# Kernel optimization log

Measured on AMD Instinct MI355X. Metric: run time of the kernel, lower is better.

## Reference

```python
import jax
jax.config.update("jax_enable_x64", True)
import jax.numpy as jnp
import numpy as np

_N = 100000
_E = 6400000


def _mix(z):
    # splitmix64 finalizer: strong per-element mixing so that summing mixed
    # neighbor colors is a (collision-resistant) commutative multiset hash.
    z = z + jnp.uint64(0x9E3779B97F4A7C15)
    z = (z ^ (z >> jnp.uint64(30))) * jnp.uint64(0xBF58476D1CE4E5B9)
    z = (z ^ (z >> jnp.uint64(27))) * jnp.uint64(0x94D049BB133111EB)
    return z ^ (z >> jnp.uint64(31))


def setup_inputs() -> dict:
    key = jax.random.key(0)
    k1, k2 = jax.random.split(key)
    x = jax.random.randint(k1, (_N,), 0, 50, dtype=jnp.int64)
    edge_index = jax.random.randint(k2, (2, _E), 0, _N, dtype=jnp.int64)
    return {"x": x, "edge_index": edge_index}


def reference(x, edge_index):
    # WL refinement: new_color[i] = ID( (x[i], multiset{x[j] : j in N(i)}) ),
    # IDs assigned in first-seen node order (matches the torch hashmap).
    # The torch code sorts neighbors before hashing, so the result depends
    # only on the neighbor MULTISET; we hash the multiset commutatively via
    # sum of splitmix64-mixed colors (collisions negligible in uint64).
    n = x.shape[0]
    row, col = edge_index[0], edge_index[1]  # neighbors of i: row[e] where col[e]==i
    neigh_hash = jax.ops.segment_sum(_mix(x[row].astype(jnp.uint64)), col,
                                     num_segments=n)  # (n,) uint64
    own = _mix(x.astype(jnp.uint64) ^ jnp.uint64(0xABCD1234DEADBEEF))
    sig = _mix(own + neigh_hash)  # (n,) per-node signature

    # Dedup + relabel in first-occurrence order (deterministic, jit-safe).
    _, inv = jnp.unique(sig, return_inverse=True, size=n, fill_value=jnp.uint64(0))
    inv = inv.reshape(-1)
    first = jax.ops.segment_min(jnp.arange(n, dtype=jnp.int64), inv,
                                num_segments=n)  # first node index per group
    rank = jnp.argsort(jnp.argsort(first))  # group -> first-seen color id
    return rank[inv].astype(jnp.int64)
```

## Files before the change

kernel.cpp:

```cpp
#include <hip/hip_runtime.h>

typedef unsigned long long u64;
typedef unsigned int u32;
typedef unsigned short u16;
typedef unsigned char u8;

#define CAP (1 << 18)
#define CAP_MASK (CAP - 1)
#define EMPTY_KEY 0xFFFFFFFFFFFFFFFFULL

#define TILE 8192
#define NXCD 8
#define NBUCK 196
#define BSHIFT 9
#define BMASK 511
#define CAPB 4608

__device__ __forceinline__ u64 mix64(u64 z) {
    z += 0x9E3779B97F4A7C15ULL;
    z = (z ^ (z >> 30)) * 0xBF58476D1CE4E5B9ULL;
    z = (z ^ (z >> 27)) * 0x94D049BB133111EBULL;
    return z ^ (z >> 31);
}

__global__ void init_ws(u64* __restrict__ neigh, u64* __restrict__ keys,
                        u32* __restrict__ firsts, u32* __restrict__ nodeslot,
                        u32* __restrict__ partials, u32* __restrict__ cursor,
                        u8* __restrict__ xb, const int* __restrict__ x, int n) {
    int i = blockIdx.x * blockDim.x + threadIdx.x;
    keys[i] = EMPTY_KEY;
    firsts[i] = 0xFFFFFFFFu;
    if (i < n) { neigh[i] = 0ULL; nodeslot[i] = 0u; xb[i] = (u8)x[i]; }
    if (i < 512) partials[i] = 0u;
    if (i < NXCD * NBUCK) cursor[i] = 0u;
}

__global__ void scatter_edges(const int* __restrict__ row, const int* __restrict__ col,
                              const u8* __restrict__ xb, u32* __restrict__ cursor,
                              u16* __restrict__ bdata, int E, int n) {
    __shared__ u32 ent[TILE];
    __shared__ u32 lcnt[NBUCK];
    __shared__ u32 lscan[NBUCK];
    __shared__ u32 lbase[NBUCK];
    __shared__ u32 s[512];
    int tid = threadIdx.x;
    int g = blockIdx.x & (NXCD - 1);
    long tile0 = (long)blockIdx.x * TILE;
    if (tid < NBUCK) lcnt[tid] = 0u;
    __syncthreads();

    u32 pk_[16];
    u32 nm = (u32)n - 1u;
    #pragma unroll
    for (int k = 0; k < 4; ++k) {
        long e0 = tile0 + (long)k * 2048 + tid * 4;
        u32 pk0 = 0xFFFFFFFFu, pk1 = 0xFFFFFFFFu, pk2 = 0xFFFFFFFFu, pk3 = 0xFFFFFFFFu;
        if (e0 < (long)E) {
            int4 r4 = *(const int4*)(row + e0);
            int4 c4 = *(const int4*)(col + e0);
            u32 c0 = min((u32)c4.x, nm), c1 = min((u32)c4.y, nm);
            u32 c2 = min((u32)c4.z, nm), c3 = min((u32)c4.w, nm);
            u32 v0 = xb[min((u32)r4.x, nm)] & 63u, v1 = xb[min((u32)r4.y, nm)] & 63u;
            u32 v2 = xb[min((u32)r4.z, nm)] & 63u, v3 = xb[min((u32)r4.w, nm)] & 63u;
            pk0 = ((c0 >> BSHIFT) << 16) | ((c0 & BMASK) << 6) | v0;
            pk1 = ((c1 >> BSHIFT) << 16) | ((c1 & BMASK) << 6) | v1;
            pk2 = ((c2 >> BSHIFT) << 16) | ((c2 & BMASK) << 6) | v2;
            pk3 = ((c3 >> BSHIFT) << 16) | ((c3 & BMASK) << 6) | v3;
            atomicAdd(&lcnt[pk0 >> 16], 1u);
            atomicAdd(&lcnt[pk1 >> 16], 1u);
            atomicAdd(&lcnt[pk2 >> 16], 1u);
            atomicAdd(&lcnt[pk3 >> 16], 1u);
        }
        pk_[k * 4 + 0] = pk0; pk_[k * 4 + 1] = pk1;
        pk_[k * 4 + 2] = pk2; pk_[k * 4 + 3] = pk3;
    }
    __syncthreads();

    u32 v = (tid < NBUCK) ? lcnt[tid] : 0u;
    s[tid] = v;
    __syncthreads();
    for (int d = 1; d < 512; d <<= 1) {
        u32 a = (tid >= d) ? s[tid - d] : 0u;
        __syncthreads();
        s[tid] += a;
        __syncthreads();
    }
    if (tid < NBUCK) {
        lscan[tid] = s[tid] - v;
        if (v) lbase[tid] = atomicAdd(&cursor[g * NBUCK + tid], v);
        lcnt[tid] = 0u;
    }
    __syncthreads();

    #pragma unroll
    for (int k = 0; k < 16; ++k) {
        u32 pk = pk_[k];
        if (pk != 0xFFFFFFFFu) {
            u32 b = pk >> 16;
            u32 pos = lscan[b] + atomicAdd(&lcnt[b], 1u);
            ent[pos] = pk;
        }
    }
    __syncthreads();

    int valid = (int)min((long)TILE, (long)E - tile0);
    for (int j = tid; j < valid; j += 512) {
        u32 pk = ent[j];
        u32 b = pk >> 16;
        u32 dst = lbase[b] + ((u32)j - lscan[b]);
        if (dst < CAPB)
            bdata[((size_t)g * NBUCK + b) * CAPB + dst] = (u16)pk;
    }
}

__global__ void bucket_reduce(const u32* __restrict__ cursor, const u16* __restrict__ bdata,
                              u64* __restrict__ neigh, int n) {
    int b = blockIdx.x;
    __shared__ u64 acc[512];
    __shared__ u64 mtab[64];
    int tid = threadIdx.x;
    if (tid < 64) mtab[tid] = mix64((u64)tid);
    if (tid < 512) acc[tid] = 0ULL;
    __syncthreads();
    for (int g = 0; g < NXCD; ++g) {
        u32 cnt = min(cursor[g * NBUCK + b], (u32)CAPB);
        const u16* seg = bdata + ((size_t)g * NBUCK + b) * CAPB;
        for (u32 i = tid; i < cnt; i += 1024) {
            u32 p = (u32)seg[i];
            atomicAdd(&acc[(p >> 6) & 511u], mtab[p & 63u]);
        }
    }
    __syncthreads();
    if (tid < 512) {
        int node = b * 512 + tid;
        if (node < n) neigh[node] = acc[tid];
    }
}

__global__ void edge_kernel(const int* __restrict__ row, const int* __restrict__ col,
                            const int* __restrict__ x, u64* __restrict__ neigh,
                            int nedges, int n) {
    int t = blockIdx.x * blockDim.x + threadIdx.x;
    int e = t * 4;
    u32 nm = (u32)n - 1u;
    if (e + 3 < nedges) {
        int4 r4 = *(const int4*)(row + e);
        int4 c4 = *(const int4*)(col + e);
        u32 r0 = min((u32)r4.x, nm), c0 = min((u32)c4.x, nm);
        u32 r1 = min((u32)r4.y, nm), c1 = min((u32)c4.y, nm);
        u32 r2 = min((u32)r4.z, nm), c2 = min((u32)c4.z, nm);
        u32 r3 = min((u32)r4.w, nm), c3 = min((u32)c4.w, nm);
        atomicAdd(&neigh[c0], mix64((u64)(u32)x[r0]));
        atomicAdd(&neigh[c1], mix64((u64)(u32)x[r1]));
        atomicAdd(&neigh[c2], mix64((u64)(u32)x[r2]));
        atomicAdd(&neigh[c3], mix64((u64)(u32)x[r3]));
    } else {
        for (int k = e; k < nedges; ++k) {
            u32 r = min((u32)row[k], nm);
            u32 c = min((u32)col[k], nm);
            atomicAdd(&neigh[c], mix64((u64)(u32)x[r]));
        }
    }
}

__global__ void sig_insert(const int* __restrict__ x, const u64* __restrict__ neigh,
                           u64* __restrict__ keys, u32* __restrict__ firsts,
                           u32* __restrict__ nodeslot, int n, int half) {
    int i = blockIdx.x * blockDim.x + threadIdx.x;
    int j = i + half;
    bool va = (i < half);
    bool vb = (j < n);
    u64 sa = 0, sb = 0;
    u32 ha = 0, hb = 0;
    if (va) {
        u64 own = mix64(((u64)(u32)x[i]) ^ 0xABCD1234DEADBEEFULL);
        sa = mix64(own + neigh[i]);
        ha = (u32)(sa ^ (sa >> 32)) & CAP_MASK;
    }
    if (vb) {
        u64 own = mix64(((u64)(u32)x[j]) ^ 0xABCD1234DEADBEEFULL);
        sb = mix64(own + neigh[j]);
        hb = (u32)(sb ^ (sb >> 32)) & CAP_MASK;
    }
    bool da = !va, db = !vb;
    for (int p = 0; p < CAP && !(da && db); ++p) {
        u64 oa, ob;
        if (!da) oa = atomicCAS(&keys[ha], EMPTY_KEY, sa);
        if (!db) ob = atomicCAS(&keys[hb], EMPTY_KEY, sb);
        if (!da) { if (oa == EMPTY_KEY || oa == sa) da = true; else ha = (ha + 1) & CAP_MASK; }
        if (!db) { if (ob == EMPTY_KEY || ob == sb) db = true; else hb = (hb + 1) & CAP_MASK; }
    }
    if (va) atomicMin(&firsts[ha], (u32)i);
    if (vb) atomicMin(&firsts[hb], (u32)j);
    if (va) nodeslot[i] = ha;
    if (vb) nodeslot[j] = hb;
}

__global__ void flags_blocksum(const u32* __restrict__ firsts, const u32* __restrict__ nodeslot,
                               u32* __restrict__ partials, int n) {
    __shared__ u32 sdata[256];
    int tid = threadIdx.x;
    int i = blockIdx.x * 256 + tid;
    u32 f = 0;
    if (i < n) f = (firsts[nodeslot[i] & CAP_MASK] == (u32)i) ? 1u : 0u;
    sdata[tid] = f;
    __syncthreads();
    for (int sft = 128; sft > 0; sft >>= 1) {
        if (tid < sft) sdata[tid] += sdata[tid + sft];
        __syncthreads();
    }
    if (tid == 0) partials[blockIdx.x] = sdata[0];
}

__global__ void scan_partials(u32* __restrict__ partials, int nb) {
    __shared__ u32 s[512];
    int t = threadIdx.x;
    u32 v = (t < nb) ? partials[t] : 0;
    s[t] = v;
    __syncthreads();
    for (int d = 1; d < 512; d <<= 1) {
        u32 a = (t >= d) ? s[t - d] : 0;
        __syncthreads();
        s[t] += a;
        __syncthreads();
    }
    if (t < nb) partials[t] = s[t] - v;
}

__global__ void assign_colors(const u32* __restrict__ firsts, const u32* __restrict__ nodeslot,
                              const u32* __restrict__ partials, u32* __restrict__ groupcolor, int n) {
    __shared__ u32 sdata[256];
    int tid = threadIdx.x;
    int i = blockIdx.x * 256 + tid;
    u32 f = 0, slot = 0;
    if (i < n) {
        slot = nodeslot[i] & CAP_MASK;
        f = (firsts[slot] == (u32)i) ? 1u : 0u;
    }
    sdata[tid] = f;
    __syncthreads();
    for (int d = 1; d < 256; d <<= 1) {
        u32 a = (tid >= d) ? sdata[tid - d] : 0;
        __syncthreads();
        sdata[tid] += a;
        __syncthreads();
    }
    u32 exc = sdata[tid] - f + partials[blockIdx.x];
    if (i < n && f) groupcolor[slot] = exc;
}

__global__ void write_out(const u32* __restrict__ nodeslot, const u32* __restrict__ groupcolor,
                          int* __restrict__ out, int n) {
    int i = blockIdx.x * blockDim.x + threadIdx.x;
    if (i < n) {
        u32 g = groupcolor[nodeslot[i] & CAP_MASK];
        g = min(g, (u32)(n - 1));
        out[i] = (int)g;
    }
}

extern "C" void kernel_launch(void* const* d_in, const int* in_sizes, int n_in,
                              void* d_out, int out_size, void* d_ws, size_t ws_size,
                              hipStream_t stream) {
    const int* x = (const int*)d_in[0];
    const int* ei = (const int*)d_in[1];
    int n = in_sizes[0];
    int E = in_sizes[1] / 2;
    const int* row = ei;
    const int* col = ei + E;

    char* base = (char*)d_ws;
    size_t off = 0;
    auto take = [&](size_t bytes) -> char* {
        char* p = base + off;
        off += (bytes + 255) & ~(size_t)255;
        return p;
    };
    u64* neigh      = (u64*)take((size_t)n * 8);
    u64* keys       = (u64*)take((size_t)CAP * 8);
    u32* firsts     = (u32*)take((size_t)CAP * 4);
    u32* nodeslot   = (u32*)take((size_t)n * 4);
    u32* partials   = (u32*)take((size_t)512 * 4);
    u8*  xb         = (u8*)take((size_t)n);
    u32* cursor     = (u32*)take((size_t)NXCD * NBUCK * 4);
    u16* bdata      = (u16*)take((size_t)NXCD * NBUCK * CAPB * 2);
    u32* groupcolor = (u32*)keys;
    bool binned = (off <= ws_size);

    int nb = (n + 255) / 256;
    int half = (n + 1) / 2;

    init_ws<<<CAP / 256, 256, 0, stream>>>(neigh, keys, firsts, nodeslot,
                                           partials, cursor, xb, x, n);
    if (binned) {
        int tiles = (E + TILE - 1) / TILE;
        scatter_edges<<<tiles, 512, 0, stream>>>(row, col, xb, cursor, bdata, E, n);
        bucket_reduce<<<NBUCK, 1024, 0, stream>>>(cursor, bdata, neigh, n);
    } else {
        edge_kernel<<<(E / 4 + 255) / 256, 256, 0, stream>>>(row, col, x, neigh, E, n);
    }
    sig_insert<<<(half + 255) / 256, 256, 0, stream>>>(x, neigh, keys, firsts, nodeslot, n, half);
    flags_blocksum<<<nb, 256, 0, stream>>>(firsts, nodeslot, partials, n);
    scan_partials<<<1, 512, 0, stream>>>(partials, nb);
    assign_colors<<<nb, 256, 0, stream>>>(firsts, nodeslot, partials, groupcolor, n);
    write_out<<<(n + 255) / 256, 256, 0, stream>>>(nodeslot, groupcolor, (int*)d_out, n);
}
```

Baseline: 161.6 us.

## Fuse tail scan into single-pass decoupled-lookback kernel and shrink scatter tiles

Replaces the three-kernel flag/blocksum, partial scan and color-assign sequence with one kernel. Each block publishes its flagged total to a status array and sums the totals of all earlier blocks by spinning on them, which removes two kernel launches. The scatter kernel moves to 256-thread blocks with 4096-edge tiles, and it reuses the rank returned by the first shared atomic instead of a second atomic pass. The spin-wait assumes earlier blocks get scheduled first; with about 391 blocks that should hold, but it is not guaranteed.

After: 161.1 us. Within noise of the previous version (-0.4%).

```diff
diff --git a/kernel.cpp b/kernel.cpp
--- a/kernel.cpp
+++ b/kernel.cpp
@@ -9,7 +9,8 @@
 #define CAP_MASK (CAP - 1)
 #define EMPTY_KEY 0xFFFFFFFFFFFFFFFFULL
 
-#define TILE 8192
+#define TILE 4096
+#define SCT 256
 #define NXCD 8
 #define NBUCK 196
 #define BSHIFT 9
@@ -25,13 +26,13 @@
 
 __global__ void init_ws(u64* __restrict__ neigh, u64* __restrict__ keys,
                         u32* __restrict__ firsts, u32* __restrict__ nodeslot,
-                        u32* __restrict__ partials, u32* __restrict__ cursor,
+                        u32* __restrict__ status, u32* __restrict__ cursor,
                         u8* __restrict__ xb, const int* __restrict__ x, int n) {
     int i = blockIdx.x * blockDim.x + threadIdx.x;
     keys[i] = EMPTY_KEY;
     firsts[i] = 0xFFFFFFFFu;
     if (i < n) { neigh[i] = 0ULL; nodeslot[i] = 0u; xb[i] = (u8)x[i]; }
-    if (i < 512) partials[i] = 0u;
+    if (i < 512) status[i] = 0u;
     if (i < NXCD * NBUCK) cursor[i] = 0u;
 }
 
@@ -42,7 +43,7 @@
     __shared__ u32 lcnt[NBUCK];
     __shared__ u32 lscan[NBUCK];
     __shared__ u32 lbase[NBUCK];
-    __shared__ u32 s[512];
+    __shared__ u32 s[SCT];
     int tid = threadIdx.x;
     int g = blockIdx.x & (NXCD - 1);
     long tile0 = (long)blockIdx.x * TILE;
@@ -50,36 +51,43 @@
     __syncthreads();
 
     u32 pk_[16];
+    u16 rk_[16];
+    u8  va_[16];
     u32 nm = (u32)n - 1u;
     #pragma unroll
     for (int k = 0; k < 4; ++k) {
-        long e0 = tile0 + (long)k * 2048 + tid * 4;
+        long e0 = tile0 + (long)k * (SCT * 4) + tid * 4;
         u32 pk0 = 0xFFFFFFFFu, pk1 = 0xFFFFFFFFu, pk2 = 0xFFFFFFFFu, pk3 = 0xFFFFFFFFu;
+        u16 r0 = 0, r1 = 0, r2 = 0, r3 = 0;
+        u8 v0 = 0, v1 = 0, v2 = 0, v3 = 0;
         if (e0 < (long)E) {
             int4 r4 = *(const int4*)(row + e0);
             int4 c4 = *(const int4*)(col + e0);
             u32 c0 = min((u32)c4.x, nm), c1 = min((u32)c4.y, nm);
             u32 c2 = min((u32)c4.z, nm), c3 = min((u32)c4.w, nm);
-            u32 v0 = xb[min((u32)r4.x, nm)] & 63u, v1 = xb[min((u32)r4.y, nm)] & 63u;
-            u32 v2 = xb[min((u32)r4.z, nm)] & 63u, v3 = xb[min((u32)r4.w, nm)] & 63u;
-            pk0 = ((c0 >> BSHIFT) << 16) | ((c0 & BMASK) << 6) | v0;
-            pk1 = ((c1 >> BSHIFT) << 16) | ((c1 & BMASK) << 6) | v1;
-            pk2 = ((c2 >> BSHIFT) << 16) | ((c2 & BMASK) << 6) | v2;
-            pk3 = ((c3 >> BSHIFT) << 16) | ((c3 & BMASK) << 6) | v3;
-            atomicAdd(&lcnt[pk0 >> 16], 1u);
-            atomicAdd(&lcnt[pk1 >> 16], 1u);
-            atomicAdd(&lcnt[pk2 >> 16], 1u);
-            atomicAdd(&lcnt[pk3 >> 16], 1u);
-        }
-        pk_[k * 4 + 0] = pk0; pk_[k * 4 + 1] = pk1;
-        pk_[k * 4 + 2] = pk2; pk_[k * 4 + 3] = pk3;
+            pk0 = ((c0 >> BSHIFT) << 16) | ((c0 & BMASK) << 6);
+            pk1 = ((c1 >> BSHIFT) << 16) | ((c1 & BMASK) << 6);
+            pk2 = ((c2 >> BSHIFT) << 16) | ((c2 & BMASK) << 6);
+            pk3 = ((c3 >> BSHIFT) << 16) | ((c3 & BMASK) << 6);
+            r0 = (u16)atomicAdd(&lcnt[pk0 >> 16], 1u);
+            r1 = (u16)atomicAdd(&lcnt[pk1 >> 16], 1u);
+            r2 = (u16)atomicAdd(&lcnt[pk2 >> 16], 1u);
+            r3 = (u16)atomicAdd(&lcnt[pk3 >> 16], 1u);
+            v0 = xb[min((u32)r4.x, nm)];
+            v1 = xb[min((u32)r4.y, nm)];
+            v2 = xb[min((u32)r4.z, nm)];
+            v3 = xb[min((u32)r4.w, nm)];
+        }
+        pk_[k*4+0] = pk0; pk_[k*4+1] = pk1; pk_[k*4+2] = pk2; pk_[k*4+3] = pk3;
+        rk_[k*4+0] = r0;  rk_[k*4+1] = r1;  rk_[k*4+2] = r2;  rk_[k*4+3] = r3;
+        va_[k*4+0] = v0;  va_[k*4+1] = v1;  va_[k*4+2] = v2;  va_[k*4+3] = v3;
     }
     __syncthreads();
 
     u32 v = (tid < NBUCK) ? lcnt[tid] : 0u;
     s[tid] = v;
     __syncthreads();
-    for (int d = 1; d < 512; d <<= 1) {
+    for (int d = 1; d < SCT; d <<= 1) {
         u32 a = (tid >= d) ? s[tid - d] : 0u;
         __syncthreads();
         s[tid] += a;
@@ -88,7 +96,6 @@
     if (tid < NBUCK) {
         lscan[tid] = s[tid] - v;
         if (v) lbase[tid] = atomicAdd(&cursor[g * NBUCK + tid], v);
-        lcnt[tid] = 0u;
     }
     __syncthreads();
 
@@ -97,14 +104,13 @@
         u32 pk = pk_[k];
         if (pk != 0xFFFFFFFFu) {
             u32 b = pk >> 16;
-            u32 pos = lscan[b] + atomicAdd(&lcnt[b], 1u);
-            ent[pos] = pk;
+            ent[lscan[b] + rk_[k]] = pk | ((u32)va_[k] & 63u);
         }
     }
     __syncthreads();
 
     int valid = (int)min((long)TILE, (long)E - tile0);
-    for (int j = tid; j < valid; j += 512) {
+    for (int j = tid; j < valid; j += SCT) {
         u32 pk = ent[j];
         u32 b = pk >> 16;
         u32 dst = lbase[b] + ((u32)j - lscan[b]);
@@ -196,42 +202,11 @@
     if (vb) nodeslot[j] = hb;
 }
 
-__global__ void flags_blocksum(const u32* __restrict__ firsts, const u32* __restrict__ nodeslot,
-                               u32* __restrict__ partials, int n) {
+__global__ void tail_assign(const u32* __restrict__ firsts, const u32* __restrict__ nodeslot,
+                            u32* __restrict__ status, u32* __restrict__ groupcolor, int n) {
     __shared__ u32 sdata[256];
-    int tid = threadIdx.x;
-    int i = blockIdx.x * 256 + tid;
-    u32 f = 0;
-    if (i < n) f = (firsts[nodeslot[i] & CAP_MASK] == (u32)i) ? 1u : 0u;
-    sdata[tid] = f;
-    __syncthreads();
-    for (int sft = 128; sft > 0; sft >>= 1) {
-        if (tid < sft) sdata[tid] += sdata[tid + sft];
-        __syncthreads();
-    }
-    if (tid == 0) partials[blockIdx.x] = sdata[0];
-}
-
-__global__ void scan_partials(u32* __restrict__ partials, int nb) {
-    __shared__ u32 s[512];
-    int t = threadIdx.x;
-    u32 v = (t < nb) ? partials[t] : 0;
-    s[t] = v;
-    __syncthreads();
-    for (int d = 1; d < 512; d <<= 1) {
-        u32 a = (t >= d) ? s[t - d] : 0;
-        __syncthreads();
-        s[t] += a;
-        __syncthreads();
-    }
-    if (t < nb) partials[t] = s[t] - v;
-}
-
-__global__ void assign_colors(const u32* __restrict__ firsts, const u32* __restrict__ nodeslot,
-                              const u32* __restrict__ partials, u32* __restrict__ groupcolor, int n) {
-    __shared__ u32 sdata[256];
-    int tid = threadIdx.x;
-    int i = blockIdx.x * 256 + tid;
+    int tid = threadIdx.x, bid = blockIdx.x;
+    int i = bid * 256 + tid;
     u32 f = 0, slot = 0;
     if (i < n) {
         slot = nodeslot[i] & CAP_MASK;
@@ -240,13 +215,32 @@
     sdata[tid] = f;
     __syncthreads();
     for (int d = 1; d < 256; d <<= 1) {
-        u32 a = (tid >= d) ? sdata[tid - d] : 0;
+        u32 a = (tid >= d) ? sdata[tid - d] : 0u;
         __syncthreads();
         sdata[tid] += a;
         __syncthreads();
     }
-    u32 exc = sdata[tid] - f + partials[blockIdx.x];
-    if (i < n && f) groupcolor[slot] = exc;
+    u32 incl = sdata[tid];
+    u32 total = sdata[255];
+    if (tid == 0) {
+        __threadfence();
+        atomicExch(&status[bid], 0x80000000u | total);
+    }
+    u32 mysum = 0;
+    for (int jb = tid; jb < bid; jb += 256) {
+        u32 v;
+        do { v = atomicAdd(&status[jb], 0u); } while (!(v & 0x80000000u));
+        mysum += v & 0x7FFFFFFFu;
+    }
+    __syncthreads();
+    sdata[tid] = mysum;
+    __syncthreads();
+    for (int sft = 128; sft > 0; sft >>= 1) {
+        if (tid < sft) sdata[tid] += sdata[tid + sft];
+        __syncthreads();
+    }
+    u32 prefix = sdata[0];
+    if (i < n && f) groupcolor[slot] = prefix + incl - 1u;
 }
 
 __global__ void write_out(const u32* __restrict__ nodeslot, const u32* __restrict__ groupcolor,
@@ -280,7 +274,7 @@
     u64* keys       = (u64*)take((size_t)CAP * 8);
     u32* firsts     = (u32*)take((size_t)CAP * 4);
     u32* nodeslot   = (u32*)take((size_t)n * 4);
-    u32* partials   = (u32*)take((size_t)512 * 4);
+    u32* status     = (u32*)take((size_t)512 * 4);
     u8*  xb         = (u8*)take((size_t)n);
     u32* cursor     = (u32*)take((size_t)NXCD * NBUCK * 4);
     u16* bdata      = (u16*)take((size_t)NXCD * NBUCK * CAPB * 2);
@@ -291,17 +285,15 @@
     int half = (n + 1) / 2;
 
     init_ws<<<CAP / 256, 256, 0, stream>>>(neigh, keys, firsts, nodeslot,
-                                           partials, cursor, xb, x, n);
+                                           status, cursor, xb, x, n);
     if (binned) {
         int tiles = (E + TILE - 1) / TILE;
-        scatter_edges<<<tiles, 512, 0, stream>>>(row, col, xb, cursor, bdata, E, n);
+        scatter_edges<<<tiles, SCT, 0, stream>>>(row, col, xb, cursor, bdata, E, n);
         bucket_reduce<<<NBUCK, 1024, 0, stream>>>(cursor, bdata, neigh, n);
     } else {
         edge_kernel<<<(E / 4 + 255) / 256, 256, 0, stream>>>(row, col, x, neigh, E, n);
     }
     sig_insert<<<(half + 255) / 256, 256, 0, stream>>>(x, neigh, keys, firsts, nodeslot, n, half);
-    flags_blocksum<<<nb, 256, 0, stream>>>(firsts, nodeslot, partials, n);
-    scan_partials<<<1, 512, 0, stream>>>(partials, nb);
-    assign_colors<<<nb, 256, 0, stream>>>(firsts, nodeslot, partials, groupcolor, n);
+    tail_assign<<<nb, 256, 0, stream>>>(firsts, nodeslot, status, groupcolor, n);
     write_out<<<(n + 255) / 256, 256, 0, stream>>>(nodeslot, groupcolor, (int*)d_out, n);
 }
```
